# Optimization experiments

Measured on AMD Instinct MI355X. Metric: run time of the kernel, lower is better.

## Reference

```python
import jax, jax.numpy as jnp
import numpy as np

N = 8192          # num_people
H = 128           # hidden_dim
ZE = 64           # zone_embed_dim
TE = 32           # temporal_embed_dim
NZ = 100          # num_zones
GRU_IN = H + ZE + TE


def _lin(k, out_d, in_d):
    kw, kb = jax.random.split(k)
    bound = 1.0 / np.sqrt(in_d)
    W = jax.random.uniform(kw, (out_d, in_d), minval=-bound, maxval=bound, dtype=jnp.float32)
    b = jax.random.uniform(kb, (out_d,), minval=-bound, maxval=bound, dtype=jnp.float32)
    return W, b


def setup_inputs() -> dict:
    key = jax.random.key(0)
    ks = jax.random.split(key, 12)
    t = jax.random.uniform(ks[0], (1,), dtype=jnp.float32)
    person_h = jax.random.normal(ks[1], (N, H), dtype=jnp.float32)
    gnn_zone_embeds = jax.random.normal(ks[2], (NZ, ZE), dtype=jnp.float32)
    W_time, b_time = _lin(ks[3], TE, 1)
    W_loc, b_loc = _lin(ks[4], NZ, H)
    Wq, bq = _lin(ks[5], H, H)
    Wk, bk = _lin(ks[6], H, H)
    Wv, bv = _lin(ks[7], H, H)
    W_merge, b_merge = _lin(ks[8], H, 2 * H)
    W_ih, b_ih = _lin(ks[9], 3 * H, GRU_IN)
    W_hh, b_hh = _lin(ks[10], 3 * H, H)
    ln_gamma = jnp.ones((H,), jnp.float32)
    ln_beta = jnp.zeros((H,), jnp.float32)
    return dict(t=t, person_h=person_h, gnn_zone_embeds=gnn_zone_embeds,
                W_time=W_time, b_time=b_time, W_loc=W_loc, b_loc=b_loc,
                Wq=Wq, bq=bq, Wk=Wk, bk=bk, Wv=Wv, bv=bv,
                W_merge=W_merge, b_merge=b_merge,
                W_ih=W_ih, b_ih=b_ih, W_hh=W_hh, b_hh=b_hh,
                ln_gamma=ln_gamma, ln_beta=ln_beta)


def reference(t, person_h, gnn_zone_embeds, W_time, b_time, W_loc, b_loc,
              Wq, bq, Wk, bk, Wv, bv, W_merge, b_merge,
              W_ih, b_ih, W_hh, b_hh, ln_gamma, ln_beta):
    n = person_h.shape[0]
    # spatial context: soft location distribution over zones
    loc_probs = jax.nn.softmax(person_h @ W_loc.T + b_loc, axis=-1)   # [N, NZ]
    spatial_context = loc_probs @ gnn_zone_embeds                     # [N, ZE]
    # leave-one-out social attention == full attention with diagonal masked
    q = person_h @ Wq.T + bq                                          # [N, H]
    k = person_h @ Wk.T + bk
    v = person_h @ Wv.T + bv
    scores = (q @ k.T) / np.sqrt(H).astype(np.float32)                # [N, N]
    diag = jnp.eye(n, dtype=bool)
    scores = jnp.where(diag, -jnp.inf, scores)
    attn = jax.nn.softmax(scores, axis=-1)
    social_context = attn @ v                                         # [N, H]
    h_interacted = jnp.concatenate([person_h, social_context], axis=-1) @ W_merge.T + b_merge
    time_context = jnp.broadcast_to(t.reshape(1, 1), (n, 1)) @ W_time.T + b_time  # [N, TE]
    gru_input = jnp.concatenate([h_interacted, spatial_context, time_context], axis=-1)
    # torch.nn.GRUCell: gates order (reset, update, new)
    gx = gru_input @ W_ih.T + b_ih                                    # [N, 3H]
    gh = person_h @ W_hh.T + b_hh
    xr, xz, xn = jnp.split(gx, 3, axis=-1)
    hr, hz, hn = jnp.split(gh, 3, axis=-1)
    r = jax.nn.sigmoid(xr + hr)
    z = jax.nn.sigmoid(xz + hz)
    ng = jnp.tanh(xn + r * hn)
    h_new = (1.0 - z) * ng + z * person_h
    d = h_new - person_h
    mu = jnp.mean(d, axis=-1, keepdims=True)
    var = jnp.var(d, axis=-1, keepdims=True)
    d = (d - mu) * jax.lax.rsqrt(var + 1e-5) * ln_gamma + ln_beta
    return d
```

## Files before the change

kernel.cpp:

```cpp
#include <hip/hip_runtime.h>


typedef __attribute__((ext_vector_type(8)))  short bf16x8;
typedef __attribute__((ext_vector_type(4)))  float f32x4;
typedef __attribute__((ext_vector_type(16))) float f32x16;
typedef __attribute__((ext_vector_type(4)))  unsigned uint4v;

#define N_P   8192
#define H_D   128
#define NCHNK 8
#define CHLEN (N_P / NCHNK)
#define KVB   64
#define NTIL  (CHLEN / KVB)
#define LDE   384

#if __has_builtin(__builtin_amdgcn_exp2f)
#define EXP2(x) __builtin_amdgcn_exp2f(x)
#else
#define EXP2(x) exp2f(x)
#endif

__device__ __forceinline__ short f2bf(float f) {
  unsigned u = __float_as_uint(f);
  u = (u + 0x7fffu + ((u >> 16) & 1u)) >> 16;
  return (short)u;
}
__device__ __forceinline__ float bf2f(short s) {
  return __uint_as_float(((unsigned)(unsigned short)s) << 16);
}

__device__ __forceinline__ int swzb(int row, int slot, int nslots) {
  return (row * nslots + (slot ^ (row & ((nslots - 1) & 7)))) << 4;
}

__device__ __forceinline__ unsigned cvtpk(float a, float b) {
  unsigned d;
  asm("v_cvt_pk_bf16_f32 %0, %1, %2" : "=v"(d) : "v"(a), "v"(b));
  return d;
}

__device__ __forceinline__ void swap32(unsigned& a, unsigned& b) {
#if __has_builtin(__builtin_amdgcn_permlane32_swap)
  auto r = __builtin_amdgcn_permlane32_swap(a, b, false, false);
  a = r[0]; b = r[1];
#else
  asm volatile("v_permlane32_swap_b32 %0, %1" : "+v"(a), "+v"(b));
#endif
}

typedef __attribute__((address_space(1))) const void GV;
typedef __attribute__((address_space(3))) void LV;
__device__ __forceinline__ void gld_lds16(const void* g, void* l) {
  __builtin_amdgcn_global_load_lds((GV*)g, (LV*)l, 16, 0, 0);
}

__constant__ const float QSCALE = 0.12751551485988857f;
#define LOG2E 1.4426950408889634f

__global__ __launch_bounds__(256) void init_kernel(
    const float* t, const float* W_time, const float* b_time,
    const float* W_loc, const float* b_loc,
    const float* Wq, const float* bq, const float* Wk, const float* bk,
    const float* Wv, const float* bv,
    const float* W_merge, const float* b_merge,
    const float* W_ih, const float* b_ih,
    const float* W_hh, const float* b_hh,
    const float* ph,
    short* W1, float* bias1, short* W_big, float* bias_big, short* PH2e) {
  const int b = blockIdx.x, tidl = threadIdx.x;
  if (b < 64) {
    int tid = b * 256 + tidl, stride = 64 * 256;
    for (int i = tid; i < 512 * 128; i += stride) {
      int r = i >> 7, k = i & 127;
      float v;
      if (r < 128)      v = Wq[r * 128 + k];
      else if (r < 256) v = Wk[(r - 128) * 128 + k];
      else if (r < 384) v = Wv[(r - 256) * 128 + k];
      else if (r < 484) v = W_loc[(r - 384) * 128 + k];
      else              v = 0.f;
      W1[i] = f2bf(v);
    }
    for (int i = tid; i < 512; i += stride) {
      float v;
      if (i < 128)      v = bq[i];
      else if (i < 256) v = bk[i - 128];
      else if (i < 384) v = bv[i - 256];
      else if (i < 484) v = b_loc[i - 384];
      else              v = 0.f;
      bias1[i] = v;
    }
  } else if (b < 576) {
    __shared__ float rowj[128];
    const int n = b - 64;
    if (tidl < 128) rowj[tidl] = (n < 384) ? W_ih[n * 224 + tidl] : 0.f;
    __syncthreads();
    {
      float acc = 0.f;
      if (n < 384) {
#pragma unroll 8
        for (int j = 0; j < 128; ++j) acc += rowj[j] * W_merge[j * 256 + tidl];
      }
      if (tidl < 128) {
        if (n < 256)      acc += W_hh[n * 128 + tidl];
        else if (n >= 384) acc = W_hh[(n - 128) * 128 + tidl];
      }
      W_big[n * 384 + tidl] = f2bf(acc);
    }
    if (tidl < 128) {
      int k2 = 256 + tidl;
      float v = 0.f;
      if (n < 384) {
        if (k2 < 320)      v = W_ih[n * 224 + 128 + (k2 - 256)];
        else if (k2 < 352) v = W_ih[n * 224 + 192 + (k2 - 320)];
      }
      W_big[n * 384 + k2] = f2bf(v);
    }
    if (tidl < 64) {
      float p = rowj[tidl] * b_merge[tidl] + rowj[tidl + 64] * b_merge[tidl + 64];
#pragma unroll
      for (int mk = 1; mk < 64; mk <<= 1) p += __shfl_xor(p, mk);
      if (tidl == 0) {
        float bb;
        if (n < 256)      bb = b_ih[n] + p + b_hh[n];
        else if (n < 384) bb = b_ih[n] + p;
        else              bb = b_hh[n - 128];
        bias_big[n] = bb;
      }
    }
  } else {
    int tid = (b - 576) * 256 + tidl, stride = 1024 * 256;
    for (int i = tid; i < N_P * H_D; i += stride) {
      int r = i >> 7, d = i & 127;
      PH2e[r * LDE + d] = f2bf(ph[i]);
    }
    const float t0 = t[0];
    for (int i = tid; i < N_P * 64; i += stride) {
      int r = i >> 6, j = i & 63;
      float v = (j < 32) ? (t0 * W_time[j] + b_time[j]) : 0.f;
      PH2e[r * LDE + 320 + j] = f2bf(v);
    }
  }
}

template <int MODE, int K>
__global__ __launch_bounds__(256, 3) void gemm64_kernel(
    const short* __restrict__ X, int ldx, const short* __restrict__ W,
    const float* __restrict__ bias,
    short* out_q, short* out_k, short* out_v, float* out_loc,
    short* out_gx) {
  __shared__ short Xl[64 * 128];
  __shared__ short Wl[128 * 128];
  const int tid = threadIdx.x;
  const int bm = blockIdx.x * 64, bn = blockIdx.y * 128;
  const int l = tid & 63, wid = tid >> 6;
  const int g = l >> 4, c = l & 15;
  const int wr = wid >> 1, wc = wid & 1;
  f32x4 acc[2][4] = {};
  constexpr int KT = K / 128;
#pragma unroll 1
  for (int kt = 0; kt < KT; ++kt) {
    const int k0 = kt * 128;
#pragma unroll
    for (int pass = 0; pass < 4; ++pass) {
      int s = tid + pass * 256;
      int row = s >> 4, p = s & 15;
      int lsl = p ^ (row & 7);
      gld_lds16(X + (size_t)(bm + row) * ldx + k0 + lsl * 8, (char*)Xl + s * 16);
    }
#pragma unroll
    for (int pass = 0; pass < 8; ++pass) {
      int s = tid + pass * 256;
      int row = s >> 4, p = s & 15;
      int lsl = p ^ (row & 7);
      gld_lds16(W + (size_t)(bn + row) * K + k0 + lsl * 8, (char*)Wl + s * 16);
    }
    __syncthreads();
#pragma unroll
    for (int kc = 0; kc < 4; ++kc) {
      bf16x8 a[2], bfr[4];
#pragma unroll
      for (int mi = 0; mi < 2; ++mi)
        a[mi] = *(const bf16x8*)((const char*)Xl + swzb(wr * 32 + mi * 16 + c, kc * 4 + g, 16));
#pragma unroll
      for (int ni = 0; ni < 4; ++ni)
        bfr[ni] = *(const bf16x8*)((const char*)Wl + swzb(wc * 64 + ni * 16 + c, kc * 4 + g, 16));
#pragma unroll
      for (int mi = 0; mi < 2; ++mi)
#pragma unroll
        for (int ni = 0; ni < 4; ++ni)
          acc[mi][ni] = __builtin_amdgcn_mfma_f32_16x16x32_bf16(a[mi], bfr[ni], acc[mi][ni], 0, 0, 0);
    }
    if (kt + 1 < KT) __syncthreads();
  }
#pragma unroll
  for (int mi = 0; mi < 2; ++mi)
#pragma unroll
    for (int ni = 0; ni < 4; ++ni)
#pragma unroll
      for (int r = 0; r < 4; ++r) {
        int row = bm + wr * 32 + mi * 16 + 4 * g + r;
        int col = bn + wc * 64 + ni * 16 + c;
        float val = acc[mi][ni][r] + bias[col];
        if constexpr (MODE == 0) {
          if (col < 128)      out_q[row * 128 + col] = f2bf(val * QSCALE);
          else if (col < 256) out_k[row * 128 + col - 128] = f2bf(val);
          else if (col < 384) out_v[row * 128 + col - 256] = f2bf(val);
          else if (col < 484) out_loc[row * 112 + col - 384] = val;
        } else {
          out_gx[row * 512 + col] = f2bf(val);
        }
      }
}

__global__ __launch_bounds__(256) void tv_spatial_kernel(const short* __restrict__ vf,
                                                         short* __restrict__ vT,
                                                         const float* __restrict__ locf,
                                                         const float* __restrict__ E,
                                                         short* __restrict__ PH2e) {
  const int b = blockIdx.x, tid = threadIdx.x;
  if (b < 1024) {
    __shared__ short T[32][40];
    int tx = tid & 31, ty = tid >> 5;
    int bi = b >> 2, bd = b & 3;
#pragma unroll
    for (int k = 0; k < 4; ++k)
      T[ty + 8 * k][tx] = vf[(bi * 32 + ty + 8 * k) * 128 + bd * 32 + tx];
    __syncthreads();
#pragma unroll
    for (int k = 0; k < 4; ++k)
      vT[(size_t)(bd * 32 + ty + 8 * k) * N_P + bi * 32 + tx] = T[tx][ty + 8 * k];
  } else {
    __shared__ float pl[4][104];
    int wid = tid >> 6, l = tid & 63;
    int row = (b - 1024) * 4 + wid;
    float v0 = locf[row * 112 + l];
    float v1 = (l + 64 < 100) ? locf[row * 112 + 64 + l] : -1e30f;
    float m = fmaxf(v0, v1);
#pragma unroll
    for (int mk = 1; mk < 64; mk <<= 1) m = fmaxf(m, __shfl_xor(m, mk));
    float p0 = EXP2((v0 - m) * LOG2E);
    float p1 = (l + 64 < 100) ? EXP2((v1 - m) * LOG2E) : 0.f;
    float s = p0 + p1;
#pragma unroll
    for (int mk = 1; mk < 64; mk <<= 1) s += __shfl_xor(s, mk);
    float inv = 1.f / s;
    pl[wid][l] = p0 * inv;
    if (l + 64 < 100) pl[wid][64 + l] = p1 * inv;
    float acc = 0.f;
#pragma unroll 4
    for (int z = 0; z < 100; ++z) acc += pl[wid][z] * E[z * 64 + l];
    PH2e[row * LDE + 256 + l] = f2bf(acc);
  }
}

__global__ __launch_bounds__(256, 2) void attn_kernel(
    const short* __restrict__ qb, const short* __restrict__ kb,
    const short* __restrict__ vT, short* __restrict__ pacc,
    float* __restrict__ pml) {
  __shared__ short Kl[2][KVB * H_D];
  __shared__ short Vl[2][H_D * KVB];
  const int tid = threadIdx.x;
  const int qbk = blockIdx.x >> 3, ch = blockIdx.x & 7;
  const int chbase = ch * CHLEN;
  const int l = tid & 63, wid = tid >> 6;
  const int c32 = l & 31, hi = l >> 5;
  const int qrow0w = qbk * 128 + wid * 32;

  char* ldsK = (char*)&Kl[0][0];
  char* ldsV = (char*)&Vl[0][0];

  auto stage = [&](int b, int tt) {
    const int off = tt * KVB;
#pragma unroll
    for (int j = 0; j < 4; ++j) {
      const int i = tid + j * 256;
      const int kr = i >> 4, ks = (i & 15) ^ (kr & 15);
      gld_lds16(kb + (size_t)(chbase + off + kr) * 128 + ks * 8,
                ldsK + b * 16384 + i * 16);
      const int vr = i >> 3, vs = (i & 7) ^ (vr & 7);
      gld_lds16(vT + (size_t)vr * N_P + chbase + off + vs * 8,
                ldsV + b * 16384 + i * 16);
    }
  };

  bf16x8 qf[8];
#pragma unroll
  for (int sl = 0; sl < 8; ++sl)
    qf[sl] = *(const bf16x8*)(qb + (size_t)(qrow0w + c32) * 128 + sl * 16 + hi * 8);

  bf16x8 ones;
#pragma unroll
  for (int j = 0; j < 8; ++j) ones[j] = (short)0x3F80;

  const int c15 = c32 & 15;
  const int kbase0 = c32 * 256;
  int koff[8];
#pragma unroll
  for (int sl = 0; sl < 8; ++sl) koff[sl] = ((2 * sl + hi) ^ c15) << 4;
  const int xh = (c32 >> 1) & 3, x0 = c32 & 1;
  const int xb = (hi ^ x0) << 4;
  int voff[4], vbase[4];
#pragma unroll
  for (int s4 = 0; s4 < 4; ++s4) voff[s4] = (s4 ^ xh) << 5;
#pragma unroll
  for (int db = 0; db < 4; ++db) vbase[db] = (db * 32 + c32) * 128 + xb;

  f32x16 acc[4] = {};
  f32x16 accl = {};
  float m = -1e30f;

  stage(0, 0);
  asm volatile("s_waitcnt vmcnt(0)" ::: "memory");
  __builtin_amdgcn_s_barrier();
  int cur = 0;

#pragma unroll 1
  for (int t = 0; t < NTIL; ++t) {
    if (t + 1 < NTIL) stage(cur ^ 1, t + 1);

    const int kv0 = chbase + t * KVB;
    const char* Kb = (const char*)&Kl[cur][0];
    const char* Vb = (const char*)&Vl[cur][0];

    f32x16 s0 = {}, s1 = {};
    __builtin_amdgcn_s_setprio(1);
#pragma unroll
    for (int sl = 0; sl < 8; ++sl) {
      bf16x8 k0 = *(const bf16x8*)(Kb + kbase0 + koff[sl]);
      bf16x8 k1 = *(const bf16x8*)(Kb + kbase0 + 8192 + koff[sl]);
      s0 = __builtin_amdgcn_mfma_f32_32x32x16_bf16(k0, qf[sl], s0, 0, 0, 0);
      s1 = __builtin_amdgcn_mfma_f32_32x32x16_bf16(k1, qf[sl], s1, 0, 0, 0);
    }
    __builtin_amdgcn_s_setprio(0);

    if (qrow0w + 32 > kv0 && qrow0w < kv0 + 64) {
      const int qr = qrow0w + c32;
#pragma unroll
      for (int r = 0; r < 16; ++r) {
        const int rowp = (r & 3) + 8 * (r >> 2) + 4 * hi;
        s0[r] = (kv0 + rowp == qr) ? -1e30f : s0[r];
        s1[r] = (kv0 + 32 + rowp == qr) ? -1e30f : s1[r];
      }
    }

    if (t == 0) {
      f32x16 mx;
#pragma unroll
      for (int r = 0; r < 16; ++r) mx[r] = fmaxf(s0[r], s1[r]);
#pragma unroll
      for (int w2 = 8; w2 >= 1; w2 >>= 1)
#pragma unroll
        for (int r = 0; r < w2; ++r) mx[r] = fmaxf(mx[r], mx[r + w2]);
      m = fmaxf(mx[0], __shfl_xor(mx[0], 32));
    }

#pragma unroll
    for (int r = 0; r < 16; ++r) s0[r] = EXP2(s0[r] - m);
#pragma unroll
    for (int r = 0; r < 16; ++r) s1[r] = EXP2(s1[r] - m);

    auto pvslice = [&](const f32x16& ss, int base, int sl4) {
      unsigned dA = cvtpk(ss[base + 0], ss[base + 1]);
      unsigned dB = cvtpk(ss[base + 2], ss[base + 3]);
      unsigned dC = cvtpk(ss[base + 4], ss[base + 5]);
      unsigned dD = cvtpk(ss[base + 6], ss[base + 7]);
      swap32(dA, dC);
      swap32(dB, dD);
      uint4v w = {dA, dB, dC, dD};
      bf16x8 pa = __builtin_bit_cast(bf16x8, w);
#pragma unroll
      for (int db = 0; db < 4; ++db) {
        bf16x8 vfr = *(const bf16x8*)(Vb + vbase[db] + voff[sl4]);
        acc[db] = __builtin_amdgcn_mfma_f32_32x32x16_bf16(pa, vfr, acc[db], 0, 0, 0);
      }
      accl = __builtin_amdgcn_mfma_f32_32x32x16_bf16(pa, ones, accl, 0, 0, 0);
    };
    __builtin_amdgcn_s_setprio(1);
    pvslice(s0, 0, 0);
    pvslice(s0, 8, 1);
    pvslice(s1, 0, 2);
    pvslice(s1, 8, 3);
    __builtin_amdgcn_s_setprio(0);

    if (t + 1 < NTIL) {
      asm volatile("s_waitcnt vmcnt(0)" ::: "memory");
      __builtin_amdgcn_s_barrier();
      asm volatile("" ::: "memory");
    }
    cur ^= 1;
  }

#pragma unroll
  for (int db = 0; db < 4; ++db)
#pragma unroll
    for (int r = 0; r < 16; ++r) {
      const int qr = qrow0w + (r & 3) + 8 * (r >> 2) + 4 * hi;
      pacc[((size_t)ch * N_P + qr) * 128 + db * 32 + c32] = f2bf(acc[db][r]);
    }
  {
    const int rr = (c32 & 3) | (((c32 >> 3) & 3) << 2);
    float own = (((c32 >> 2) & 1) == hi) ? accl[rr] : 0.f;
    float lv = own + __shfl_xor(own, 32);
    if (hi == 0) {
      const int qr = qrow0w + c32;
      pml[((size_t)ch * N_P + qr) * 2]     = m;
      pml[((size_t)ch * N_P + qr) * 2 + 1] = lv;
    }
  }
}

__global__ __launch_bounds__(256) void combine_kernel(const short* __restrict__ pacc,
                                                      const float* __restrict__ pml,
                                                      short* __restrict__ PH2e) {
  int tid = threadIdx.x;
  int row = blockIdx.x * 2 + (tid >> 7);
  int d = tid & 127;
  float mv[NCHNK], lv[NCHNK], M = -1e30f;
#pragma unroll
  for (int cc = 0; cc < NCHNK; ++cc) {
    mv[cc] = pml[(cc * N_P + row) * 2];
    lv[cc] = pml[(cc * N_P + row) * 2 + 1];
    M = fmaxf(M, mv[cc]);
  }
  float L = 0.f, O = 0.f;
#pragma unroll
  for (int cc = 0; cc < NCHNK; ++cc) {
    float w = EXP2(mv[cc] - M);
    L += lv[cc] * w;
    O += bf2f(pacc[((size_t)cc * N_P + row) * 128 + d]) * w;
  }
  PH2e[row * LDE + 128 + d] = f2bf(O / L);
}

__global__ __launch_bounds__(256) void final_kernel(const short* __restrict__ gxs,
                                                    const float* __restrict__ ph,
                                                    const float* __restrict__ gamma,
                                                    const float* __restrict__ beta,
                                                    float* __restrict__ out) {
  int tid = threadIdx.x, wid = tid >> 6, l = tid & 63;
  int row = blockIdx.x * 4 + wid;
  float dd[2];
#pragma unroll
  for (int half = 0; half < 2; ++half) {
    int d = l + 64 * half;
    float h  = ph[row * 128 + d];
    float sr = bf2f(gxs[row * 512 + d]);
    float sz = bf2f(gxs[row * 512 + 128 + d]);
    float xn = bf2f(gxs[row * 512 + 256 + d]);
    float hn = bf2f(gxs[row * 512 + 384 + d]);
    float r = 1.f / (1.f + EXP2(-LOG2E * sr));
    float z = 1.f / (1.f + EXP2(-LOG2E * sz));
    float a = xn + r * hn;
    float ng = 1.f - 2.f / (1.f + EXP2(2.f * LOG2E * a));
    dd[half] = (1.f - z) * (ng - h);
  }
  float s = dd[0] + dd[1], ss = dd[0] * dd[0] + dd[1] * dd[1];
#pragma unroll
  for (int mk = 1; mk < 64; mk <<= 1) {
    s += __shfl_xor(s, mk);
    ss += __shfl_xor(ss, mk);
  }
  float mu = s * (1.f / 128.f);
  float var = ss * (1.f / 128.f) - mu * mu;
  float rs = rsqrtf(var + 1e-5f);
#pragma unroll
  for (int half = 0; half < 2; ++half) {
    int d = l + 64 * half;
    out[row * 128 + d] = (dd[half] - mu) * rs * gamma[d] + beta[d];
  }
}

extern "C" void kernel_launch(void* const* d_in, const int* in_sizes, int n_in,
                              void* d_out, int out_size, void* d_ws, size_t ws_size,
                              hipStream_t stream) {
  const float* t       = (const float*)d_in[0];
  const float* ph      = (const float*)d_in[1];
  const float* E       = (const float*)d_in[2];
  const float* W_time  = (const float*)d_in[3];
  const float* b_time  = (const float*)d_in[4];
  const float* W_loc   = (const float*)d_in[5];
  const float* b_loc   = (const float*)d_in[6];
  const float* Wq      = (const float*)d_in[7];
  const float* bq      = (const float*)d_in[8];
  const float* Wk      = (const float*)d_in[9];
  const float* bk      = (const float*)d_in[10];
  const float* Wv      = (const float*)d_in[11];
  const float* bv      = (const float*)d_in[12];
  const float* W_merge = (const float*)d_in[13];
  const float* b_merge = (const float*)d_in[14];
  const float* W_ih    = (const float*)d_in[15];
  const float* b_ih    = (const float*)d_in[16];
  const float* W_hh    = (const float*)d_in[17];
  const float* b_hh    = (const float*)d_in[18];
  const float* gamma   = (const float*)d_in[19];
  const float* beta    = (const float*)d_in[20];
  float* out = (float*)d_out;

  char* w = (char*)d_ws;
  auto alloc = [&](size_t bytes) {
    char* p = w;
    w += (bytes + 255) & ~(size_t)255;
    return p;
  };
  short* W1      = (short*)alloc(512 * 128 * 2);
  float* bias1   = (float*)alloc(512 * 4);
  short* W_big   = (short*)alloc(512 * 384 * 2);
  float* bias_big= (float*)alloc(512 * 4);
  short* PH2e    = (short*)alloc((size_t)N_P * LDE * 2);
  short* qbuf    = (short*)alloc((size_t)N_P * 128 * 2);
  short* kbuf    = (short*)alloc((size_t)N_P * 128 * 2);
  short* vf      = (short*)alloc((size_t)N_P * 128 * 2);
  short* vT      = (short*)alloc((size_t)128 * N_P * 2);
  float* locf    = (float*)alloc((size_t)N_P * 112 * 4);
  short* gxs     = (short*)alloc((size_t)N_P * 512 * 2);
  short* pacc    = (short*)alloc((size_t)NCHNK * N_P * 128 * 2);
  float* pml     = (float*)alloc((size_t)NCHNK * N_P * 2 * 4);

  init_kernel<<<1600, 256, 0, stream>>>(t, W_time, b_time, W_loc, b_loc, Wq, bq,
                                        Wk, bk, Wv, bv, W_merge, b_merge,
                                        W_ih, b_ih, W_hh, b_hh, ph,
                                        W1, bias1, W_big, bias_big, PH2e);
  gemm64_kernel<0, 128><<<dim3(128, 4), 256, 0, stream>>>(
      PH2e, LDE, W1, bias1, qbuf, kbuf, vf, locf, nullptr);
  tv_spatial_kernel<<<3072, 256, 0, stream>>>(vf, vT, locf, E, PH2e);
  attn_kernel<<<512, 256, 0, stream>>>(qbuf, kbuf, vT, pacc, pml);
  combine_kernel<<<4096, 256, 0, stream>>>(pacc, pml, PH2e);
  gemm64_kernel<2, 384><<<dim3(128, 4), 256, 0, stream>>>(
      PH2e, LDE, W_big, bias_big, nullptr, nullptr, nullptr, nullptr, gxs);
  final_kernel<<<2048, 256, 0, stream>>>(gxs, ph, gamma, beta, out);
}
```

Measured before the change: 92.36 us.

## Fuse V transpose into projection GEMM epilogue and merge spatial softmax into combine

The projection GEMM now writes V directly in transposed layout through an LDS staging tile, which removes the separate transpose pass and the intermediate row-major V buffer. The spatial softmax-and-embedding work moves out of the old transpose kernel into the attention combine kernel as extra blocks, so one launch is dropped. The cost is an extra LDS round trip and barrier in the V-column blocks of the GEMM, and the combine launch becomes larger.

```diff
diff --git a/kernel.cpp b/kernel.cpp
--- a/kernel.cpp
+++ b/kernel.cpp
@@ -146,7 +146,7 @@
 __global__ __launch_bounds__(256, 3) void gemm64_kernel(
     const short* __restrict__ X, int ldx, const short* __restrict__ W,
     const float* __restrict__ bias,
-    short* out_q, short* out_k, short* out_v, float* out_loc,
+    short* out_q, short* out_k, short* out_vT, float* out_loc,
     short* out_gx) {
   __shared__ short Xl[64 * 128];
   __shared__ short Wl[128 * 128];
@@ -192,64 +192,53 @@
     }
     if (kt + 1 < KT) __syncthreads();
   }
-#pragma unroll
-  for (int mi = 0; mi < 2; ++mi)
-#pragma unroll
-    for (int ni = 0; ni < 4; ++ni)
-#pragma unroll
-      for (int r = 0; r < 4; ++r) {
-        int row = bm + wr * 32 + mi * 16 + 4 * g + r;
-        int col = bn + wc * 64 + ni * 16 + c;
-        float val = acc[mi][ni][r] + bias[col];
-        if constexpr (MODE == 0) {
-          if (col < 128)      out_q[row * 128 + col] = f2bf(val * QSCALE);
-          else if (col < 256) out_k[row * 128 + col - 128] = f2bf(val);
-          else if (col < 384) out_v[row * 128 + col - 256] = f2bf(val);
-          else if (col < 484) out_loc[row * 112 + col - 384] = val;
-        } else {
-          out_gx[row * 512 + col] = f2bf(val);
+  if constexpr (MODE == 0) {
+    if (blockIdx.y == 2) {
+      __syncthreads();
+      short* T = Wl;
+#pragma unroll
+      for (int mi = 0; mi < 2; ++mi)
+#pragma unroll
+        for (int ni = 0; ni < 4; ++ni)
+#pragma unroll
+          for (int r = 0; r < 4; ++r) {
+            int rl = wr * 32 + mi * 16 + 4 * g + r;
+            int cl = wc * 64 + ni * 16 + c;
+            T[rl * 130 + cl] = f2bf(acc[mi][ni][r] + bias[256 + cl]);
+          }
+      __syncthreads();
+#pragma unroll
+      for (int pass = 0; pass < 32; ++pass) {
+        int d = pass * 4 + (tid >> 6);
+        int j = tid & 63;
+        out_vT[(size_t)d * N_P + bm + j] = T[j * 130 + d];
+      }
+    } else {
+#pragma unroll
+      for (int mi = 0; mi < 2; ++mi)
+#pragma unroll
+        for (int ni = 0; ni < 4; ++ni)
+#pragma unroll
+          for (int r = 0; r < 4; ++r) {
+            int row = bm + wr * 32 + mi * 16 + 4 * g + r;
+            int col = bn + wc * 64 + ni * 16 + c;
+            float val = acc[mi][ni][r] + bias[col];
+            if (col < 128)      out_q[row * 128 + col] = f2bf(val * QSCALE);
+            else if (col < 256) out_k[row * 128 + col - 128] = f2bf(val);
+            else if (col >= 384 && col < 484) out_loc[row * 112 + col - 384] = val;
+          }
+    }
+  } else {
+#pragma unroll
+    for (int mi = 0; mi < 2; ++mi)
+#pragma unroll
+      for (int ni = 0; ni < 4; ++ni)
+#pragma unroll
+        for (int r = 0; r < 4; ++r) {
+          int row = bm + wr * 32 + mi * 16 + 4 * g + r;
+          int col = bn + wc * 64 + ni * 16 + c;
+          out_gx[row * 512 + col] = f2bf(acc[mi][ni][r] + bias[col]);
         }
-      }
-}
-
-__global__ __launch_bounds__(256) void tv_spatial_kernel(const short* __restrict__ vf,
-                                                         short* __restrict__ vT,
-                                                         const float* __restrict__ locf,
-                                                         const float* __restrict__ E,
-                                                         short* __restrict__ PH2e) {
-  const int b = blockIdx.x, tid = threadIdx.x;
-  if (b < 1024) {
-    __shared__ short T[32][40];
-    int tx = tid & 31, ty = tid >> 5;
-    int bi = b >> 2, bd = b & 3;
-#pragma unroll
-    for (int k = 0; k < 4; ++k)
-      T[ty + 8 * k][tx] = vf[(bi * 32 + ty + 8 * k) * 128 + bd * 32 + tx];
-    __syncthreads();
-#pragma unroll
-    for (int k = 0; k < 4; ++k)
-      vT[(size_t)(bd * 32 + ty + 8 * k) * N_P + bi * 32 + tx] = T[tx][ty + 8 * k];
-  } else {
-    __shared__ float pl[4][104];
-    int wid = tid >> 6, l = tid & 63;
-    int row = (b - 1024) * 4 + wid;
-    float v0 = locf[row * 112 + l];
-    float v1 = (l + 64 < 100) ? locf[row * 112 + 64 + l] : -1e30f;
-    float m = fmaxf(v0, v1);
-#pragma unroll
-    for (int mk = 1; mk < 64; mk <<= 1) m = fmaxf(m, __shfl_xor(m, mk));
-    float p0 = EXP2((v0 - m) * LOG2E);
-    float p1 = (l + 64 < 100) ? EXP2((v1 - m) * LOG2E) : 0.f;
-    float s = p0 + p1;
-#pragma unroll
-    for (int mk = 1; mk < 64; mk <<= 1) s += __shfl_xor(s, mk);
-    float inv = 1.f / s;
-    pl[wid][l] = p0 * inv;
-    if (l + 64 < 100) pl[wid][64 + l] = p1 * inv;
-    float acc = 0.f;
-#pragma unroll 4
-    for (int z = 0; z < 100; ++z) acc += pl[wid][z] * E[z * 64 + l];
-    PH2e[row * LDE + 256 + l] = f2bf(acc);
   }
 }
 
@@ -409,27 +398,51 @@
   }
 }
 
-__global__ __launch_bounds__(256) void combine_kernel(const short* __restrict__ pacc,
-                                                      const float* __restrict__ pml,
-                                                      short* __restrict__ PH2e) {
-  int tid = threadIdx.x;
-  int row = blockIdx.x * 2 + (tid >> 7);
-  int d = tid & 127;
-  float mv[NCHNK], lv[NCHNK], M = -1e30f;
-#pragma unroll
-  for (int cc = 0; cc < NCHNK; ++cc) {
-    mv[cc] = pml[(cc * N_P + row) * 2];
-    lv[cc] = pml[(cc * N_P + row) * 2 + 1];
-    M = fmaxf(M, mv[cc]);
-  }
-  float L = 0.f, O = 0.f;
-#pragma unroll
-  for (int cc = 0; cc < NCHNK; ++cc) {
-    float w = EXP2(mv[cc] - M);
-    L += lv[cc] * w;
-    O += bf2f(pacc[((size_t)cc * N_P + row) * 128 + d]) * w;
-  }
-  PH2e[row * LDE + 128 + d] = f2bf(O / L);
+__global__ __launch_bounds__(256) void combine_spatial_kernel(
+    const short* __restrict__ pacc, const float* __restrict__ pml,
+    const float* __restrict__ locf, const float* __restrict__ E,
+    short* __restrict__ PH2e) {
+  const int b = blockIdx.x, tid = threadIdx.x;
+  if (b < 4096) {
+    int row = b * 2 + (tid >> 7);
+    int d = tid & 127;
+    float mv[NCHNK], lv[NCHNK], M = -1e30f;
+#pragma unroll
+    for (int cc = 0; cc < NCHNK; ++cc) {
+      mv[cc] = pml[(cc * N_P + row) * 2];
+      lv[cc] = pml[(cc * N_P + row) * 2 + 1];
+      M = fmaxf(M, mv[cc]);
+    }
+    float L = 0.f, O = 0.f;
+#pragma unroll
+    for (int cc = 0; cc < NCHNK; ++cc) {
+      float w = EXP2(mv[cc] - M);
+      L += lv[cc] * w;
+      O += bf2f(pacc[((size_t)cc * N_P + row) * 128 + d]) * w;
+    }
+    PH2e[row * LDE + 128 + d] = f2bf(O / L);
+  } else {
+    __shared__ float pl[4][104];
+    int wid = tid >> 6, l = tid & 63;
+    int row = (b - 4096) * 4 + wid;
+    float v0 = locf[row * 112 + l];
+    float v1 = (l + 64 < 100) ? locf[row * 112 + 64 + l] : -1e30f;
+    float m = fmaxf(v0, v1);
+#pragma unroll
+    for (int mk = 1; mk < 64; mk <<= 1) m = fmaxf(m, __shfl_xor(m, mk));
+    float p0 = EXP2((v0 - m) * LOG2E);
+    float p1 = (l + 64 < 100) ? EXP2((v1 - m) * LOG2E) : 0.f;
+    float s = p0 + p1;
+#pragma unroll
+    for (int mk = 1; mk < 64; mk <<= 1) s += __shfl_xor(s, mk);
+    float inv = 1.f / s;
+    pl[wid][l] = p0 * inv;
+    if (l + 64 < 100) pl[wid][64 + l] = p1 * inv;
+    float acc = 0.f;
+#pragma unroll 4
+    for (int z = 0; z < 100; ++z) acc += pl[wid][z] * E[z * 64 + l];
+    PH2e[row * LDE + 256 + l] = f2bf(acc);
+  }
 }
 
 __global__ __launch_bounds__(256) void final_kernel(const short* __restrict__ gxs,
@@ -509,7 +522,6 @@
   short* PH2e    = (short*)alloc((size_t)N_P * LDE * 2);
   short* qbuf    = (short*)alloc((size_t)N_P * 128 * 2);
   short* kbuf    = (short*)alloc((size_t)N_P * 128 * 2);
-  short* vf      = (short*)alloc((size_t)N_P * 128 * 2);
   short* vT      = (short*)alloc((size_t)128 * N_P * 2);
   float* locf    = (float*)alloc((size_t)N_P * 112 * 4);
   short* gxs     = (short*)alloc((size_t)N_P * 512 * 2);
@@ -521,10 +533,9 @@
                                         W_ih, b_ih, W_hh, b_hh, ph,
                                         W1, bias1, W_big, bias_big, PH2e);
   gemm64_kernel<0, 128><<<dim3(128, 4), 256, 0, stream>>>(
-      PH2e, LDE, W1, bias1, qbuf, kbuf, vf, locf, nullptr);
-  tv_spatial_kernel<<<3072, 256, 0, stream>>>(vf, vT, locf, E, PH2e);
+      PH2e, LDE, W1, bias1, qbuf, kbuf, vT, locf, nullptr);
   attn_kernel<<<512, 256, 0, stream>>>(qbuf, kbuf, vT, pacc, pml);
-  combine_kernel<<<4096, 256, 0, stream>>>(pacc, pml, PH2e);
+  combine_spatial_kernel<<<6144, 256, 0, stream>>>(pacc, pml, locf, E, PH2e);
   gemm64_kernel<2, 384><<<dim3(128, 4), 256, 0, stream>>>(
       PH2e, LDE, W_big, bias_big, nullptr, nullptr, nullptr, nullptr, gxs);
   final_kernel<<<2048, 256, 0, stream>>>(gxs, ph, gamma, beta, out);
```

Result: faster. 88.43 us (-4.3%).
